# Kernel optimization log

Measured on AMD Instinct MI355X. Metric: run time of the kernel, lower is better.

## Reference

```python
import jax, jax.numpy as jnp
import numpy as np

STRIDES = {"feat1": 4, "feat2": 8, "feat3": 16}
ROI_SIZES = {"feat1": 28, "feat2": 14, "feat3": 7}
SAMPLING_RATIO = 2


def roi_align(feat, rois, out_size, spatial_scale, ratio):
    """torchvision roi_align with aligned=True, fixed sampling_ratio.
    feat: (B,C,H,W); rois: (N,5) [batch_idx,x1,y1,x2,y2]. Returns (N,C,P,P)."""
    B, C, H, W = feat.shape
    bidx = rois[:, 0].astype(jnp.int32)
    # aligned=True: half-pixel offset
    x1 = rois[:, 1] * spatial_scale - 0.5
    y1 = rois[:, 2] * spatial_scale - 0.5
    x2 = rois[:, 3] * spatial_scale - 0.5
    y2 = rois[:, 4] * spatial_scale - 0.5
    bin_h = (y2 - y1) / out_size
    bin_w = (x2 - x1) / out_size
    # per-bin sampling grid offsets: (P, r)
    grid = jnp.arange(out_size, dtype=feat.dtype)[:, None] + \
        (jnp.arange(ratio, dtype=feat.dtype)[None, :] + 0.5) / ratio
    ys = y1[:, None, None] + grid[None] * bin_h[:, None, None]  # (N,P,ry)
    xs = x1[:, None, None] + grid[None] * bin_w[:, None, None]  # (N,P,rx)
    yy = ys[:, :, :, None, None]  # (N,P,ry,1,1)
    xx = xs[:, None, None, :, :]  # (N,1,1,P,rx)
    valid = (yy > -1.0) & (yy < H) & (xx > -1.0) & (xx < W)
    yc = jnp.clip(yy, 0.0, H - 1.0)
    xc = jnp.clip(xx, 0.0, W - 1.0)
    y0 = jnp.floor(yc).astype(jnp.int32)
    x0 = jnp.floor(xc).astype(jnp.int32)
    y1i = jnp.minimum(y0 + 1, H - 1)
    x1i = jnp.minimum(x0 + 1, W - 1)
    ly = yc - y0
    lx = xc - x0
    hy = 1.0 - ly
    hx = 1.0 - lx
    b = bidx[:, None, None, None, None]  # (N,1,1,1,1)

    def gather(yi, xi):
        # advanced indexing -> (N,P,ry,P,rx,C)
        return feat[b, :, yi, xi]

    v = ((hy * hx)[..., None] * gather(y0, x0)
         + (hy * lx)[..., None] * gather(y0, x1i)
         + (ly * hx)[..., None] * gather(y1i, x0)
         + (ly * lx)[..., None] * gather(y1i, x1i))
    v = jnp.where(valid[..., None], v, 0.0)
    out = v.mean(axis=(2, 4))  # average over sampling grid -> (N,P,P,C)
    return jnp.transpose(out, (0, 3, 1, 2))  # (N,C,P,P)


def setup_inputs() -> dict:
    key = jax.random.key(0)
    ks = jax.random.split(key, 6)
    B, C, N, IMG = 2, 256, 128, 1024
    feat1 = jax.random.normal(ks[0], (B, C, 256, 256), jnp.float32)
    feat2 = jax.random.normal(ks[1], (B, C, 128, 128), jnp.float32)
    feat3 = jax.random.normal(ks[2], (B, C, 64, 64), jnp.float32)
    bidx = jax.random.randint(ks[3], (N,), 0, B).astype(jnp.float32)
    xy1 = jax.random.uniform(ks[4], (N, 2), jnp.float32, 0.0, IMG - 64.0)
    wh = jax.random.uniform(ks[5], (N, 2), jnp.float32, 16.0, 320.0)
    xy2 = jnp.minimum(xy1 + wh, IMG - 1.0)
    rois = jnp.concatenate(
        [bidx[:, None], xy1[:, :1], xy1[:, 1:], xy2[:, :1], xy2[:, 1:]], axis=1)
    return {"feat1": feat1, "feat2": feat2, "feat3": feat3, "rois": rois}


def reference(feat1, feat2, feat3, rois):
    feats = {"feat1": feat1, "feat2": feat2, "feat3": feat3}
    return tuple(
        roi_align(feats[k], rois, ROI_SIZES[k], 1.0 / STRIDES[k], SAMPLING_RATIO)
        for k in ("feat1", "feat2", "feat3"))
```

## Files before the change

### kernel.cpp

```cpp
#include <hip/hip_runtime.h>

#define C_CH 256

__global__ __launch_bounds__(256) void nchw_to_nhwc(
    const float* __restrict__ in, float* __restrict__ out, int HW)
{
    __shared__ float lds[64 * 64];
    int ct = blockIdx.y & 3;
    int b  = blockIdx.y >> 2;
    int hw0 = blockIdx.x << 6;
    int c0  = ct << 6;
    const float* ip = in  + (size_t)b * C_CH * HW;
    float*       op = out + (size_t)b * HW * C_CH;

    int t   = threadIdx.x;
    int q   = t & 15;
    int r0  = t >> 4;

#pragma unroll
    for (int k = 0; k < 4; ++k) {
        int c_local = r0 + (k << 4);
        const float4 v = *reinterpret_cast<const float4*>(
            ip + (size_t)(c0 + c_local) * HW + hw0 + (q << 2));
#pragma unroll
        for (int i = 0; i < 4; ++i) {
            int hw_local = (q << 2) + i;
            lds[(hw_local << 6) + ((c_local + hw_local) & 63)] = ((const float*)&v)[i];
        }
    }
    __syncthreads();
#pragma unroll
    for (int k = 0; k < 4; ++k) {
        int hw_local = r0 + (k << 4);
        float4 v;
#pragma unroll
        for (int j = 0; j < 4; ++j) {
            int c_local = (q << 2) + j;
            ((float*)&v)[j] = lds[(hw_local << 6) + ((c_local + hw_local) & 63)];
        }
        *reinterpret_cast<float4*>(
            op + (size_t)(hw0 + hw_local) * C_CH + c0 + (q << 2)) = v;
    }
}

__device__ __forceinline__ void woff16(
    int ph, int pw, float y1, float x1, float bin_h, float bin_w,
    int H, int W, int c4, float* __restrict__ w, int* __restrict__ off)
{
    const float Hm1 = (float)(H - 1), Wm1 = (float)(W - 1);
    const float Hf = (float)H, Wf = (float)W;
#pragma unroll
    for (int iy = 0; iy < 2; ++iy) {
        float gy = (float)ph + (iy ? 0.75f : 0.25f);
        float yy = fmaf(gy, bin_h, y1);
        bool vy = (yy > -1.0f) && (yy < Hf);
        float yc = fminf(fmaxf(yy, 0.0f), Hm1);
        float y0f = floorf(yc);
        int   y0  = (int)y0f;
        float ly  = yc - y0f, hy = 1.0f - ly;
        int   y1i = min(y0 + 1, H - 1);
        int ro0 = y0 * W, ro1 = y1i * W;
#pragma unroll
        for (int ix = 0; ix < 2; ++ix) {
            float gx = (float)pw + (ix ? 0.75f : 0.25f);
            float xx = fmaf(gx, bin_w, x1);
            bool v = vy && (xx > -1.0f) && (xx < Wf);
            float xc = fminf(fmaxf(xx, 0.0f), Wm1);
            float x0f = floorf(xc);
            int   x0  = (int)x0f;
            float lx  = xc - x0f, hx = 1.0f - lx;
            int   x1i = min(x0 + 1, W - 1);
            float q = v ? 0.25f : 0.0f;
            int s = ((iy << 1) + ix) << 2;
            w[s + 0] = hy * hx * q;  off[s + 0] = ((ro0 + x0 ) << 8) + c4;
            w[s + 1] = hy * lx * q;  off[s + 1] = ((ro0 + x1i) << 8) + c4;
            w[s + 2] = ly * hx * q;  off[s + 2] = ((ro1 + x0 ) << 8) + c4;
            w[s + 3] = ly * lx * q;  off[s + 3] = ((ro1 + x1i) << 8) + c4;
        }
    }
}

template<int P, int POS>
__global__ __launch_bounds__(256, 3) void roi_gather_nhwc(
    const float* __restrict__ nhwc, const float* __restrict__ rois,
    float* __restrict__ out, int H, int W, float scale, int N)
{
    constexpr int PITCH = 260;
    constexpr int NB = (P * P) / POS;
    __shared__ float lds[POS * PITCH];

    const int G = N * NB;
    int bid = blockIdx.x;
    int virt = (G % 8 == 0) ? ((bid & 7) * (G >> 3) + (bid >> 3)) : bid;
    int n  = virt / NB;
    int rb = virt - n * NB;
    int ph0 = rb * (POS / P);

    const int lane = threadIdx.x & 63;
    const int wid  = threadIdx.x >> 6;
    const int c4   = lane << 2;

    const float* r = rois + n * 5;
    const int b = (int)r[0];
    const float x1 = fmaf(r[1], scale, -0.5f);
    const float y1 = fmaf(r[2], scale, -0.5f);
    const float x2 = fmaf(r[3], scale, -0.5f);
    const float y2 = fmaf(r[4], scale, -0.5f);
    const float bin_h = (y2 - y1) * (1.0f / P);
    const float bin_w = (x2 - x1) * (1.0f / P);
    const float* fb = nhwc + (size_t)b * H * W * C_CH;

    for (int pos = wid; pos < POS; pos += 4) {
        int ph = ph0 + pos / P;
        int pw = pos % P;

        float w[16];
        int   off[16];
        woff16(ph, pw, y1, x1, bin_h, bin_w, H, W, c4, w, off);

        float4 v[16];
#pragma unroll
        for (int m = 0; m < 16; ++m)
            v[m] = *reinterpret_cast<const float4*>(fb + (size_t)(unsigned)off[m]);
        __builtin_amdgcn_sched_barrier(0);

        float4 acc = {0.f, 0.f, 0.f, 0.f};
#pragma unroll
        for (int m = 0; m < 16; ++m) {
            acc.x = fmaf(w[m], v[m].x, acc.x);
            acc.y = fmaf(w[m], v[m].y, acc.y);
            acc.z = fmaf(w[m], v[m].z, acc.z);
            acc.w = fmaf(w[m], v[m].w, acc.w);
        }
        int slot = ((c4 >> 2) ^ (pos & 7)) << 2;
        *reinterpret_cast<float4*>(&lds[pos * PITCH + slot]) = acc;
    }
    __syncthreads();

    const size_t obase = (size_t)n * C_CH * (P * P) + (size_t)ph0 * P;
    if constexpr (P != 7) {
        constexpr int K4 = POS / 4;
        for (int i = threadIdx.x; i < C_CH * K4; i += 256) {
            int c  = i / K4;
            int k4 = i - c * K4;
            float4 o;
#pragma unroll
            for (int j = 0; j < 4; ++j) {
                int pos = (k4 << 2) + j;
                ((float*)&o)[j] = lds[pos * PITCH + ((((c >> 2) ^ (pos & 7)) << 2) | (c & 3))];
            }
            *reinterpret_cast<float4*>(out + obase + (size_t)c * (P * P) + (k4 << 2)) = o;
        }
    } else {
        for (int i = threadIdx.x; i < C_CH * POS; i += 256) {
            int c   = i / POS;
            int pos = i - c * POS;
            out[obase + (size_t)c * (P * P) + pos] =
                lds[pos * PITCH + ((((c >> 2) ^ (pos & 7)) << 2) | (c & 3))];
        }
    }
}

template<int P, int CPT>
__global__ __launch_bounds__(256) void roi_align_direct(
    const float* __restrict__ feat, const float* __restrict__ rois,
    float* __restrict__ out, int N, int H, int W, float scale)
{
    constexpr int CG = C_CH / CPT;
    int tid = blockIdx.x * blockDim.x + threadIdx.x;
    int total = N * CG * P * P;
    if (tid >= total) return;

    int pw = tid % P;
    int t  = tid / P;
    int ph = t % P;
    t /= P;
    int cg = t % CG;
    int n  = t / CG;

    const float* r = rois + n * 5;
    int b = (int)r[0];
    float x1 = fmaf(r[1], scale, -0.5f);
    float y1 = fmaf(r[2], scale, -0.5f);
    float x2 = fmaf(r[3], scale, -0.5f);
    float y2 = fmaf(r[4], scale, -0.5f);
    float bin_h = (y2 - y1) * (1.0f / P);
    float bin_w = (x2 - x1) * (1.0f / P);

    float acc[CPT];
#pragma unroll
    for (int j = 0; j < CPT; ++j) acc[j] = 0.0f;

    const int HW = H * W;
    const float* fp = feat + ((size_t)b * C_CH + (size_t)cg * CPT) * HW;

    float w[16]; int off[16];
    woff16(ph, pw, y1, x1, bin_h, bin_w, H, W, 0, w, off);
#pragma unroll
    for (int m = 0; m < 16; ++m) {
        int sp = off[m] >> 8;
#pragma unroll
        for (int j = 0; j < CPT; ++j)
            acc[j] = fmaf(w[m], fp[(size_t)j * HW + sp], acc[j]);
    }

    float* op = out + (((size_t)n * C_CH + (size_t)cg * CPT) * P + ph) * P + pw;
#pragma unroll
    for (int j = 0; j < CPT; ++j) op[(size_t)j * P * P] = acc[j];
}

extern "C" void kernel_launch(void* const* d_in, const int* in_sizes, int n_in,
                              void* d_out, int out_size, void* d_ws, size_t ws_size,
                              hipStream_t stream) {
    const float* feat1 = (const float*)d_in[0];
    const float* feat2 = (const float*)d_in[1];
    const float* feat3 = (const float*)d_in[2];
    const float* rois  = (const float*)d_in[3];
    const int N = in_sizes[3] / 5;

    float* out1 = (float*)d_out;
    float* out2 = out1 + (size_t)N * C_CH * 28 * 28;
    float* out3 = out2 + (size_t)N * C_CH * 14 * 14;

    const size_t e1 = (size_t)2 * C_CH * 256 * 256;
    const size_t e2 = (size_t)2 * C_CH * 128 * 128;
    const size_t e3 = (size_t)2 * C_CH * 64 * 64;

    size_t off = 0;
    float* t1 = nullptr; float* t2 = nullptr; float* t3 = nullptr;
    if (off + e1 * 4 <= ws_size) { t1 = (float*)((char*)d_ws + off); off += e1 * 4; }
    if (off + e2 * 4 <= ws_size) { t2 = (float*)((char*)d_ws + off); off += e2 * 4; }
    if (off + e3 * 4 <= ws_size) { t3 = (float*)((char*)d_ws + off); off += e3 * 4; }

    if (t1) nchw_to_nhwc<<<dim3(65536 / 64, 8), 256, 0, stream>>>(feat1, t1, 65536);
    if (t2) nchw_to_nhwc<<<dim3(16384 / 64, 8), 256, 0, stream>>>(feat2, t2, 16384);
    if (t3) nchw_to_nhwc<<<dim3( 4096 / 64, 8), 256, 0, stream>>>(feat3, t3,  4096);

    if (t1) {
        roi_gather_nhwc<28, 28><<<N * 28, 256, 0, stream>>>(t1, rois, out1, 256, 256, 0.25f, N);
    } else {
        int total = N * (C_CH / 4) * 28 * 28;
        roi_align_direct<28, 4><<<(total + 255) / 256, 256, 0, stream>>>(feat1, rois, out1, N, 256, 256, 0.25f);
    }
    if (t2) {
        roi_gather_nhwc<14, 28><<<N * 7, 256, 0, stream>>>(t2, rois, out2, 128, 128, 0.125f, N);
    } else {
        int total = N * (C_CH / 4) * 14 * 14;
        roi_align_direct<14, 4><<<(total + 255) / 256, 256, 0, stream>>>(feat2, rois, out2, N, 128, 128, 0.125f);
    }
    if (t3) {
        roi_gather_nhwc<7, 49><<<N * 1, 256, 0, stream>>>(t3, rois, out3, 64, 64, 0.0625f, N);
    } else {
        int total = N * (C_CH / 4) * 7 * 7;
        roi_align_direct<7, 4><<<(total + 255) / 256, 256, 0, stream>>>(feat3, rois, out3, N, 64, 64, 0.0625f);
    }
}
```

Baseline: 423.3 us.

## Factor bilinear sampling into separable merged row/column taps and skip zero-weight loads

```diff
diff --git a/kernel.cpp b/kernel.cpp
--- a/kernel.cpp
+++ b/kernel.cpp
@@ -43,41 +43,32 @@
     }
 }
 
-__device__ __forceinline__ void woff16(
-    int ph, int pw, float y1, float x1, float bin_h, float bin_w,
-    int H, int W, int c4, float* __restrict__ w, int* __restrict__ off)
-{
-    const float Hm1 = (float)(H - 1), Wm1 = (float)(W - 1);
-    const float Hf = (float)H, Wf = (float)W;
-#pragma unroll
-    for (int iy = 0; iy < 2; ++iy) {
-        float gy = (float)ph + (iy ? 0.75f : 0.25f);
-        float yy = fmaf(gy, bin_h, y1);
-        bool vy = (yy > -1.0f) && (yy < Hf);
-        float yc = fminf(fmaxf(yy, 0.0f), Hm1);
-        float y0f = floorf(yc);
-        int   y0  = (int)y0f;
-        float ly  = yc - y0f, hy = 1.0f - ly;
-        int   y1i = min(y0 + 1, H - 1);
-        int ro0 = y0 * W, ro1 = y1i * W;
-#pragma unroll
-        for (int ix = 0; ix < 2; ++ix) {
-            float gx = (float)pw + (ix ? 0.75f : 0.25f);
-            float xx = fmaf(gx, bin_w, x1);
-            bool v = vy && (xx > -1.0f) && (xx < Wf);
-            float xc = fminf(fmaxf(xx, 0.0f), Wm1);
-            float x0f = floorf(xc);
-            int   x0  = (int)x0f;
-            float lx  = xc - x0f, hx = 1.0f - lx;
-            int   x1i = min(x0 + 1, W - 1);
-            float q = v ? 0.25f : 0.0f;
-            int s = ((iy << 1) + ix) << 2;
-            w[s + 0] = hy * hx * q;  off[s + 0] = ((ro0 + x0 ) << 8) + c4;
-            w[s + 1] = hy * lx * q;  off[s + 1] = ((ro0 + x1i) << 8) + c4;
-            w[s + 2] = ly * hx * q;  off[s + 2] = ((ro1 + x0 ) << 8) + c4;
-            w[s + 3] = ly * lx * q;  off[s + 3] = ((ro1 + x1i) << 8) + c4;
-        }
-    }
+__device__ __forceinline__ void taps4(
+    int p, float lo, float bin, int L, float* __restrict__ Wt, int& i0)
+{
+    const float Lf = (float)L, Lm1 = (float)(L - 1);
+    float sa = fmaf((float)p + 0.25f, bin, lo);
+    float sb = fmaf((float)p + 0.75f, bin, lo);
+    float va = (sa > -1.0f && sa < Lf) ? 1.0f : 0.0f;
+    float vb = (sb > -1.0f && sb < Lf) ? 1.0f : 0.0f;
+    float ca = fminf(fmaxf(sa, 0.0f), Lm1);
+    float cb = fminf(fmaxf(sb, 0.0f), Lm1);
+    float fa = floorf(ca), fb_ = floorf(cb);
+    int ia0 = (int)fa, ib0 = (int)fb_;
+    float la = ca - fa, ha = 1.0f - la;
+    float lb = cb - fb_, hb = 1.0f - lb;
+    int ia1 = min(ia0 + 1, L - 1);
+    int ib1 = min(ib0 + 1, L - 1);
+    i0 = ia0;
+    int ka1 = ia1 - ia0;
+    int kb0 = ib0 - ia0;
+    int kb1 = ib1 - ia0;
+    float wa0 = ha * va, wa1 = la * va;
+    float wb0 = hb * vb, wb1 = lb * vb;
+    Wt[0] = wa0 + (ka1 == 0 ? wa1 : 0.f) + (kb0 == 0 ? wb0 : 0.f) + (kb1 == 0 ? wb1 : 0.f);
+    Wt[1] =       (ka1 == 1 ? wa1 : 0.f) + (kb0 == 1 ? wb0 : 0.f) + (kb1 == 1 ? wb1 : 0.f);
+    Wt[2] =                                (kb0 == 2 ? wb0 : 0.f) + (kb1 == 2 ? wb1 : 0.f);
+    Wt[3] =                                                         (kb1 == 3 ? wb1 : 0.f);
 }
 
 template<int P, int POS>
@@ -114,50 +105,41 @@
         int ph = ph0 + pos / P;
         int pw = pos % P;
 
-        float w[16];
-        int   off[16];
-        woff16(ph, pw, y1, x1, bin_h, bin_w, H, W, c4, w, off);
-
-        float4 v[16];
-#pragma unroll
-        for (int m = 0; m < 16; ++m)
-            v[m] = *reinterpret_cast<const float4*>(fb + (size_t)(unsigned)off[m]);
-        __builtin_amdgcn_sched_barrier(0);
+        float WY[4], WX[4];
+        int r0, c0;
+        taps4(ph, y1, bin_h, H, WY, r0);
+        taps4(pw, x1, bin_w, W, WX, c0);
+        WX[0] *= 0.25f; WX[1] *= 0.25f; WX[2] *= 0.25f; WX[3] *= 0.25f;
 
         float4 acc = {0.f, 0.f, 0.f, 0.f};
-#pragma unroll
-        for (int m = 0; m < 16; ++m) {
-            acc.x = fmaf(w[m], v[m].x, acc.x);
-            acc.y = fmaf(w[m], v[m].y, acc.y);
-            acc.z = fmaf(w[m], v[m].z, acc.z);
-            acc.w = fmaf(w[m], v[m].w, acc.w);
-        }
-        int slot = ((c4 >> 2) ^ (pos & 7)) << 2;
-        *reinterpret_cast<float4*>(&lds[pos * PITCH + slot]) = acc;
+        const unsigned base = (unsigned)(r0 * W + c0);
+#pragma unroll
+        for (int k = 0; k < 4; ++k) {
+            if (WY[k] != 0.0f) {
+                const unsigned rowb = base + (unsigned)(k * W);
+#pragma unroll
+                for (int j = 0; j < 4; ++j) {
+                    if (WX[j] != 0.0f) {
+                        const float4 v = *reinterpret_cast<const float4*>(
+                            fb + ((size_t)((rowb + j) << 8) + c4));
+                        const float wt = WY[k] * WX[j];
+                        acc.x = fmaf(wt, v.x, acc.x);
+                        acc.y = fmaf(wt, v.y, acc.y);
+                        acc.z = fmaf(wt, v.z, acc.z);
+                        acc.w = fmaf(wt, v.w, acc.w);
+                    }
+                }
+            }
+        }
+        *reinterpret_cast<float4*>(&lds[pos * PITCH + c4]) = acc;
     }
     __syncthreads();
 
     const size_t obase = (size_t)n * C_CH * (P * P) + (size_t)ph0 * P;
-    if constexpr (P != 7) {
-        constexpr int K4 = POS / 4;
-        for (int i = threadIdx.x; i < C_CH * K4; i += 256) {
-            int c  = i / K4;
-            int k4 = i - c * K4;
-            float4 o;
-#pragma unroll
-            for (int j = 0; j < 4; ++j) {
-                int pos = (k4 << 2) + j;
-                ((float*)&o)[j] = lds[pos * PITCH + ((((c >> 2) ^ (pos & 7)) << 2) | (c & 3))];
-            }
-            *reinterpret_cast<float4*>(out + obase + (size_t)c * (P * P) + (k4 << 2)) = o;
-        }
-    } else {
-        for (int i = threadIdx.x; i < C_CH * POS; i += 256) {
-            int c   = i / POS;
-            int pos = i - c * POS;
-            out[obase + (size_t)c * (P * P) + pos] =
-                lds[pos * PITCH + ((((c >> 2) ^ (pos & 7)) << 2) | (c & 3))];
-        }
+    for (int i = threadIdx.x; i < C_CH * POS; i += 256) {
+        int c   = i / POS;
+        int pos = i - c * POS;
+        out[obase + (size_t)c * (P * P) + pos] = lds[pos * PITCH + c];
     }
 }
 
@@ -194,14 +176,27 @@
     const int HW = H * W;
     const float* fp = feat + ((size_t)b * C_CH + (size_t)cg * CPT) * HW;
 
-    float w[16]; int off[16];
-    woff16(ph, pw, y1, x1, bin_h, bin_w, H, W, 0, w, off);
-#pragma unroll
-    for (int m = 0; m < 16; ++m) {
-        int sp = off[m] >> 8;
-#pragma unroll
-        for (int j = 0; j < CPT; ++j)
-            acc[j] = fmaf(w[m], fp[(size_t)j * HW + sp], acc[j]);
+    float WY[4], WX[4];
+    int r0, c0;
+    taps4(ph, y1, bin_h, H, WY, r0);
+    taps4(pw, x1, bin_w, W, WX, c0);
+    WX[0] *= 0.25f; WX[1] *= 0.25f; WX[2] *= 0.25f; WX[3] *= 0.25f;
+
+#pragma unroll
+    for (int k = 0; k < 4; ++k) {
+        if (WY[k] != 0.0f) {
+            int rowb = (r0 + k) * W + c0;
+#pragma unroll
+            for (int m = 0; m < 4; ++m) {
+                if (WX[m] != 0.0f) {
+                    float wt = WY[k] * WX[m];
+                    int sp = rowb + m;
+#pragma unroll
+                    for (int j = 0; j < CPT; ++j)
+                        acc[j] = fmaf(wt, fp[(size_t)j * HW + sp], acc[j]);
+                }
+            }
+        }
     }
 
     float* op = out + (((size_t)n * C_CH + (size_t)cg * CPT) * P + ph) * P + pw;
```

After: 487.4 us. 15.2% more time.

## Store NHWC feature copies in bf16 to halve transpose writes and gather reads

Applied to the files above, without the earlier changes.

```diff
diff --git a/kernel.cpp b/kernel.cpp
--- a/kernel.cpp
+++ b/kernel.cpp
@@ -2,8 +2,14 @@
 
 #define C_CH 256
 
-__global__ __launch_bounds__(256) void nchw_to_nhwc(
-    const float* __restrict__ in, float* __restrict__ out, int HW)
+__device__ __forceinline__ unsigned short f2bf_rne(float f) {
+    unsigned u = __float_as_uint(f);
+    u += 0x7FFFu + ((u >> 16) & 1u);
+    return (unsigned short)(u >> 16);
+}
+
+__global__ __launch_bounds__(256) void nchw_to_nhwc_bf16(
+    const float* __restrict__ in, unsigned short* __restrict__ out, int HW)
 {
     __shared__ float lds[64 * 64];
     int ct = blockIdx.y & 3;
@@ -11,11 +17,11 @@
     int hw0 = blockIdx.x << 6;
     int c0  = ct << 6;
     const float* ip = in  + (size_t)b * C_CH * HW;
-    float*       op = out + (size_t)b * HW * C_CH;
-
-    int t   = threadIdx.x;
-    int q   = t & 15;
-    int r0  = t >> 4;
+    unsigned short* op = out + (size_t)b * HW * C_CH;
+
+    int t  = threadIdx.x;
+    int q  = t & 15;
+    int r0 = t >> 4;
 
 #pragma unroll
     for (int k = 0; k < 4; ++k) {
@@ -32,14 +38,15 @@
 #pragma unroll
     for (int k = 0; k < 4; ++k) {
         int hw_local = r0 + (k << 4);
-        float4 v;
+        ushort4 o;
 #pragma unroll
         for (int j = 0; j < 4; ++j) {
             int c_local = (q << 2) + j;
-            ((float*)&v)[j] = lds[(hw_local << 6) + ((c_local + hw_local) & 63)];
-        }
-        *reinterpret_cast<float4*>(
-            op + (size_t)(hw0 + hw_local) * C_CH + c0 + (q << 2)) = v;
+            ((unsigned short*)&o)[j] =
+                f2bf_rne(lds[(hw_local << 6) + ((c_local + hw_local) & 63)]);
+        }
+        *reinterpret_cast<ushort4*>(
+            op + (size_t)(hw0 + hw_local) * C_CH + c0 + (q << 2)) = o;
     }
 }
 
@@ -81,8 +88,8 @@
 }
 
 template<int P, int POS>
-__global__ __launch_bounds__(256, 3) void roi_gather_nhwc(
-    const float* __restrict__ nhwc, const float* __restrict__ rois,
+__global__ __launch_bounds__(256, 4) void roi_gather_nhwc(
+    const unsigned short* __restrict__ nhwc, const float* __restrict__ rois,
     float* __restrict__ out, int H, int W, float scale, int N)
 {
     constexpr int PITCH = 260;
@@ -108,7 +115,7 @@
     const float y2 = fmaf(r[4], scale, -0.5f);
     const float bin_h = (y2 - y1) * (1.0f / P);
     const float bin_w = (x2 - x1) * (1.0f / P);
-    const float* fb = nhwc + (size_t)b * H * W * C_CH;
+    const unsigned short* fb = nhwc + (size_t)b * H * W * C_CH;
 
     for (int pos = wid; pos < POS; pos += 4) {
         int ph = ph0 + pos / P;
@@ -118,46 +125,32 @@
         int   off[16];
         woff16(ph, pw, y1, x1, bin_h, bin_w, H, W, c4, w, off);
 
-        float4 v[16];
+        uint2 v[16];
 #pragma unroll
         for (int m = 0; m < 16; ++m)
-            v[m] = *reinterpret_cast<const float4*>(fb + (size_t)(unsigned)off[m]);
-        __builtin_amdgcn_sched_barrier(0);
+            v[m] = *reinterpret_cast<const uint2*>(fb + (size_t)(unsigned)off[m]);
 
         float4 acc = {0.f, 0.f, 0.f, 0.f};
 #pragma unroll
         for (int m = 0; m < 16; ++m) {
-            acc.x = fmaf(w[m], v[m].x, acc.x);
-            acc.y = fmaf(w[m], v[m].y, acc.y);
-            acc.z = fmaf(w[m], v[m].z, acc.z);
-            acc.w = fmaf(w[m], v[m].w, acc.w);
-        }
-        int slot = ((c4 >> 2) ^ (pos & 7)) << 2;
-        *reinterpret_cast<float4*>(&lds[pos * PITCH + slot]) = acc;
+            float f0 = __uint_as_float(v[m].x << 16);
+            float f1 = __uint_as_float(v[m].x & 0xFFFF0000u);
+            float f2 = __uint_as_float(v[m].y << 16);
+            float f3 = __uint_as_float(v[m].y & 0xFFFF0000u);
+            acc.x = fmaf(w[m], f0, acc.x);
+            acc.y = fmaf(w[m], f1, acc.y);
+            acc.z = fmaf(w[m], f2, acc.z);
+            acc.w = fmaf(w[m], f3, acc.w);
+        }
+        *reinterpret_cast<float4*>(&lds[pos * PITCH + c4]) = acc;
     }
     __syncthreads();
 
     const size_t obase = (size_t)n * C_CH * (P * P) + (size_t)ph0 * P;
-    if constexpr (P != 7) {
-        constexpr int K4 = POS / 4;
-        for (int i = threadIdx.x; i < C_CH * K4; i += 256) {
-            int c  = i / K4;
-            int k4 = i - c * K4;
-            float4 o;
-#pragma unroll
-            for (int j = 0; j < 4; ++j) {
-                int pos = (k4 << 2) + j;
-                ((float*)&o)[j] = lds[pos * PITCH + ((((c >> 2) ^ (pos & 7)) << 2) | (c & 3))];
-            }
-            *reinterpret_cast<float4*>(out + obase + (size_t)c * (P * P) + (k4 << 2)) = o;
-        }
-    } else {
-        for (int i = threadIdx.x; i < C_CH * POS; i += 256) {
-            int c   = i / POS;
-            int pos = i - c * POS;
-            out[obase + (size_t)c * (P * P) + pos] =
-                lds[pos * PITCH + ((((c >> 2) ^ (pos & 7)) << 2) | (c & 3))];
-        }
+    for (int i = threadIdx.x; i < C_CH * POS; i += 256) {
+        int c   = i / POS;
+        int pos = i - c * POS;
+        out[obase + (size_t)c * (P * P) + pos] = lds[pos * PITCH + c];
     }
 }
 
@@ -227,14 +220,14 @@
     const size_t e3 = (size_t)2 * C_CH * 64 * 64;
 
     size_t off = 0;
-    float* t1 = nullptr; float* t2 = nullptr; float* t3 = nullptr;
-    if (off + e1 * 4 <= ws_size) { t1 = (float*)((char*)d_ws + off); off += e1 * 4; }
-    if (off + e2 * 4 <= ws_size) { t2 = (float*)((char*)d_ws + off); off += e2 * 4; }
-    if (off + e3 * 4 <= ws_size) { t3 = (float*)((char*)d_ws + off); off += e3 * 4; }
-
-    if (t1) nchw_to_nhwc<<<dim3(65536 / 64, 8), 256, 0, stream>>>(feat1, t1, 65536);
-    if (t2) nchw_to_nhwc<<<dim3(16384 / 64, 8), 256, 0, stream>>>(feat2, t2, 16384);
-    if (t3) nchw_to_nhwc<<<dim3( 4096 / 64, 8), 256, 0, stream>>>(feat3, t3,  4096);
+    unsigned short* t1 = nullptr; unsigned short* t2 = nullptr; unsigned short* t3 = nullptr;
+    if (off + e1 * 2 <= ws_size) { t1 = (unsigned short*)((char*)d_ws + off); off += e1 * 2; }
+    if (off + e2 * 2 <= ws_size) { t2 = (unsigned short*)((char*)d_ws + off); off += e2 * 2; }
+    if (off + e3 * 2 <= ws_size) { t3 = (unsigned short*)((char*)d_ws + off); off += e3 * 2; }
+
+    if (t1) nchw_to_nhwc_bf16<<<dim3(65536 / 64, 8), 256, 0, stream>>>(feat1, t1, 65536);
+    if (t2) nchw_to_nhwc_bf16<<<dim3(16384 / 64, 8), 256, 0, stream>>>(feat2, t2, 16384);
+    if (t3) nchw_to_nhwc_bf16<<<dim3( 4096 / 64, 8), 256, 0, stream>>>(feat3, t3,  4096);
 
     if (t1) {
         roi_gather_nhwc<28, 28><<<N * 28, 256, 0, stream>>>(t1, rois, out1, 256, 256, 0.25f, N);
```

Result: faster. 359.6 us (-15.0%).
